# Kernel optimization log

Hardware: AMD Instinct MI355X
Metric: run time of the kernel (lower is better)

The kernel has to match this reference:

```python
import jax, jax.numpy as jnp
import numpy as np

B, H, S, D = 65536, 512, 256, 64  # batch, hidden_dim, memory_slots, slot_size


def setup_inputs() -> dict:
    key = jax.random.key(0)
    ks = jax.random.split(key, 8)
    scale = 1.0 / np.sqrt(H)
    return {
        "query": jax.random.normal(ks[0], (B, H), jnp.float32),
        "content": jax.random.normal(ks[1], (B, H), jnp.float32),
        "memory": jax.random.normal(ks[2], (S, D), jnp.float32),
        "memory_age": jax.random.uniform(ks[3], (S,), jnp.float32, 0.0, 30.0),
        "W_read": jax.random.normal(ks[4], (H, S), jnp.float32) * scale,
        "b_read": jnp.zeros((S,), jnp.float32),
        "W_write": jax.random.normal(ks[5], (H, S), jnp.float32) * scale,
        "b_write": jnp.zeros((S,), jnp.float32),
        "W_content": jax.random.normal(ks[6], (H, D), jnp.float32) * scale,
        "b_content": jnp.zeros((D,), jnp.float32),
    }


def reference(query, content, memory, memory_age,
              W_read, b_read, W_write, b_write, W_content, b_content):
    # ---- read: attention-based addressing over memory slots ----
    read_weights = jax.nn.softmax(query @ W_read + b_read, axis=-1)      # [B, S]
    read_content = read_weights @ memory                                  # [B, D]

    # ---- write: consolidation dynamics (vectorized per-slot EMA) ----
    write_weights = jax.nn.softmax(query @ W_write + b_write, axis=-1)   # [B, S]
    processed_content = content @ W_content + b_content                   # [B, D]
    w_mean = write_weights.mean(axis=0)                                    # [S]
    c_mean = processed_content.mean(axis=0)                                # [D]

    active = w_mean > 0.01                                                 # [S] bool
    consolidation = jax.nn.sigmoid(memory_age * 0.1)                       # [S]
    # effective blend factor; zero for inactive slots (slot left untouched)
    alpha = jnp.where(active, w_mean * consolidation, 0.0)[:, None]        # [S, 1]
    new_memory = (1.0 - alpha) * memory + alpha * c_mean[None, :]          # [S, D]
    new_age = memory_age + active.astype(memory_age.dtype)                 # [S]

    return read_content, new_memory, new_age
```

## Files before the change

kernel.cpp:

```cpp
#include <hip/hip_runtime.h>
#include <hip/hip_bf16.h>


typedef short short8 __attribute__((ext_vector_type(8)));
typedef float floatx4 __attribute__((ext_vector_type(4)));

#define H_DIM 512
#define BM 32

#define WS_WT    0
#define WS_MEMT  589824
#define WS_BFULL 622592
#define WS_WSUM  624896
#define WS_CSUM  625920

__device__ __forceinline__ unsigned short f2b(float f) {
  unsigned u = __float_as_uint(f);
  u += 0x7fffu + ((u >> 16) & 1u);
  return (unsigned short)(u >> 16);
}
__device__ __forceinline__ float b2f(unsigned short h) {
  return __uint_as_float(((unsigned)h) << 16);
}
__device__ __forceinline__ unsigned cvt2(float x, float y) {
  union { __hip_bfloat162 h; unsigned u; } c;
  c.h = __float22bfloat162_rn(make_float2(x, y));
  return c.u;
}

__global__ void drcn_init(const float* __restrict__ W_read, const float* __restrict__ W_write,
                          const float* __restrict__ W_content, const float* __restrict__ b_read,
                          const float* __restrict__ b_write, const float* __restrict__ b_content,
                          const float* __restrict__ memory,
                          unsigned short* __restrict__ Wt, unsigned short* __restrict__ memT,
                          float* __restrict__ bfull, float* __restrict__ w_sum,
                          float* __restrict__ c_sum) {
  int idx = blockIdx.x * 256 + threadIdx.x;
  if (idx < 294912) {
    int n = idx >> 9, k = idx & 511;
    float v;
    if (n < 256)      v = W_read[k * 256 + n];
    else if (n < 512) v = W_write[k * 256 + (n - 256)];
    else              v = W_content[k * 64 + (n - 512)];
    Wt[idx] = f2b(v);
  } else if (idx < 311296) {
    int i = idx - 294912;
    int d = i >> 8, s = i & 255;
    memT[i] = f2b(memory[s * 64 + d]);
  } else if (idx < 311872) {
    int n = idx - 311296;
    bfull[n] = (n < 256) ? b_read[n] : (n < 512 ? b_write[n - 256] : b_content[n - 512]);
  } else if (idx < 312192) {
    int i = idx - 311872;
    if (i < 256) w_sum[i] = 0.0f; else c_sum[i - 256] = 0.0f;
  }
}

__global__ __launch_bounds__(256, 2) void drcn_main(
    const float* __restrict__ query, const float* __restrict__ content,
    const unsigned short* __restrict__ Wt, const float* __restrict__ bfull,
    const unsigned short* __restrict__ memT, float* __restrict__ w_sum,
    float* __restrict__ c_sum, float* __restrict__ out) {
  __shared__ __align__(16) char smem[65536];
  unsigned short* lg = (unsigned short*)smem;
  float* cs = (float*)(smem + 37376);
  float* cp = (float*)(smem + 38400);

  const int t = threadIdx.x;
  const int wv = t >> 6;
  const int ln = t & 63;
  const int ln15 = ln & 15;
  const int quad = ln >> 4;
  const int m0 = blockIdx.x * BM;

  const unsigned short* bp[9];
  short8 breg[9];
  #pragma unroll
  for (int j = 0; j < 9; j++) {
    bp[j] = Wt + (size_t)(((wv * 9 + j) * 16 + ln15) * 512 + quad * 8);
    breg[j] = *(const short8*)bp[j];
  }

  float bias[9];
  #pragma unroll
  for (int j = 0; j < 9; j++) bias[j] = bfull[(wv * 9 + j) * 16 + ln15];

  {
    const int row = t >> 3, jj = t & 7;
    const float* qrow = query   + (size_t)(m0 + row) * H_DIM;
    const float* crow = content + (size_t)(m0 + row) * H_DIM;
    char* aqr = smem + row * 1024;
    char* acr = smem + 32768 + row * 1024;
    #pragma unroll
    for (int i = 0; i < 8; i++) {
      const int g = jj + i * 8;
      const int sw = ((g ^ (row & 7)) << 4);
      float4 f0 = *(const float4*)(qrow + g * 8);
      float4 f1 = *(const float4*)(qrow + g * 8 + 4);
      float4 g0 = *(const float4*)(crow + g * 8);
      float4 g1 = *(const float4*)(crow + g * 8 + 4);
      short8 s; unsigned* su = (unsigned*)&s;
      su[0] = cvt2(f0.x, f0.y); su[1] = cvt2(f0.z, f0.w);
      su[2] = cvt2(f1.x, f1.y); su[3] = cvt2(f1.z, f1.w);
      *(short8*)(aqr + sw) = s;
      short8 sc; unsigned* cu = (unsigned*)&sc;
      cu[0] = cvt2(g0.x, g0.y); cu[1] = cvt2(g0.z, g0.w);
      cu[2] = cvt2(g1.x, g1.y); cu[3] = cvt2(g1.z, g1.w);
      *(short8*)(acr + sw) = sc;
    }
  }

  floatx4 acc[2][9];
  #pragma unroll
  for (int mt = 0; mt < 2; mt++)
    #pragma unroll
    for (int j = 0; j < 9; j++) {
      floatx4 z = {0.0f, 0.0f, 0.0f, 0.0f};
      acc[mt][j] = z;
    }

  __syncthreads();

  #pragma unroll 2
  for (int it = 0; it < 16; ++it) {
    short8 aq[2], ac[2];
    #pragma unroll
    for (int mt = 0; mt < 2; mt++) {
      const int row = mt * 16 + ln15;
      const int sw = row * 1024 + ((((it * 4 + quad) ^ (row & 7))) << 4);
      aq[mt] = *(const short8*)(smem + sw);
      ac[mt] = *(const short8*)(smem + 32768 + sw);
    }
    #pragma unroll
    for (int j = 0; j < 9; j++) {
      const int nt = wv * 9 + j;
      #pragma unroll
      for (int mt = 0; mt < 2; mt++) {
        short8 a = (nt >= 32) ? ac[mt] : aq[mt];
        acc[mt][j] = __builtin_amdgcn_mfma_f32_16x16x32_bf16(a, breg[j], acc[mt][j], 0, 0, 0);
      }
      if (it < 15)
        breg[j] = *(const short8*)(bp[j] + (it + 1) * 32);
    }
  }
  __syncthreads();

  #pragma unroll
  for (int j = 0; j < 9; j++) {
    int n = (wv * 9 + j) * 16 + ln15;
    #pragma unroll
    for (int mt = 0; mt < 2; mt++) {
      #pragma unroll
      for (int r = 0; r < 4; r++) {
        int row = mt * 16 + quad * 4 + r;
        lg[row * 584 + n] = f2b(acc[mt][j][r] + bias[j]);
      }
    }
  }
  cs[t] = 0.0f;
  if (t < 64) cp[t] = 0.0f;
  __syncthreads();

  const int r = t >> 3, c = t & 7;
  unsigned short* lrow = lg + r * 584;

  {
    float v[32];
    #pragma unroll
    for (int ch = 0; ch < 4; ch++) {
      short8 u = *(const short8*)(lrow + c * 32 + ch * 8);
      #pragma unroll
      for (int e = 0; e < 8; e++) v[ch * 8 + e] = b2f((unsigned short)u[e]);
    }
    float mx = -3.0e38f;
    #pragma unroll
    for (int i = 0; i < 32; i++) mx = fmaxf(mx, v[i]);
    mx = fmaxf(mx, __shfl_xor(mx, 1));
    mx = fmaxf(mx, __shfl_xor(mx, 2));
    mx = fmaxf(mx, __shfl_xor(mx, 4));
    float sm = 0.0f;
    #pragma unroll
    for (int i = 0; i < 32; i++) { v[i] = __expf(v[i] - mx); sm += v[i]; }
    sm += __shfl_xor(sm, 1);
    sm += __shfl_xor(sm, 2);
    sm += __shfl_xor(sm, 4);
    float inv = 1.0f / sm;
    #pragma unroll
    for (int ch = 0; ch < 4; ch++) {
      short8 u;
      #pragma unroll
      for (int e = 0; e < 8; e++) u[e] = (short)f2b(v[ch * 8 + e] * inv);
      *(short8*)(lrow + c * 32 + ch * 8) = u;
    }
  }
  {
    float v[32];
    #pragma unroll
    for (int ch = 0; ch < 4; ch++) {
      short8 u = *(const short8*)(lrow + 256 + c * 32 + ch * 8);
      #pragma unroll
      for (int e = 0; e < 8; e++) v[ch * 8 + e] = b2f((unsigned short)u[e]);
    }
    float mx = -3.0e38f;
    #pragma unroll
    for (int i = 0; i < 32; i++) mx = fmaxf(mx, v[i]);
    mx = fmaxf(mx, __shfl_xor(mx, 1));
    mx = fmaxf(mx, __shfl_xor(mx, 2));
    mx = fmaxf(mx, __shfl_xor(mx, 4));
    float sm = 0.0f;
    #pragma unroll
    for (int i = 0; i < 32; i++) { v[i] = __expf(v[i] - mx); sm += v[i]; }
    sm += __shfl_xor(sm, 1);
    sm += __shfl_xor(sm, 2);
    sm += __shfl_xor(sm, 4);
    float inv = 1.0f / sm;
    #pragma unroll
    for (int i = 0; i < 32; i++) {
      float p = v[i] * inv;
      p += __shfl_xor(p, 8);
      p += __shfl_xor(p, 16);
      p += __shfl_xor(p, 32);
      v[i] = p;
    }
    if (ln < 8) {
      #pragma unroll
      for (int i = 0; i < 32; i++) atomicAdd(&cs[c * 32 + i], v[i]);
    }
  }
  {
    float v[8];
    short8 u = *(const short8*)(lrow + 512 + c * 8);
    #pragma unroll
    for (int e = 0; e < 8; e++) v[e] = b2f((unsigned short)u[e]);
    #pragma unroll
    for (int e = 0; e < 8; e++) {
      float p = v[e];
      p += __shfl_xor(p, 8);
      p += __shfl_xor(p, 16);
      p += __shfl_xor(p, 32);
      v[e] = p;
    }
    if (ln < 8) {
      #pragma unroll
      for (int e = 0; e < 8; e++) atomicAdd(&cp[c * 8 + e], v[e]);
    }
  }
  __syncthreads();

  {
    int mt = wv & 1, nd0 = (wv >> 1) * 2;
    floatx4 ra[2];
    floatx4 z = {0.0f, 0.0f, 0.0f, 0.0f};
    ra[0] = z; ra[1] = z;
    #pragma unroll
    for (int ks = 0; ks < 8; ks++) {
      int s0 = ks * 32 + quad * 8;
      short8 a = *(const short8*)(lg + (mt * 16 + ln15) * 584 + s0);
      #pragma unroll
      for (int dt = 0; dt < 2; dt++) {
        short8 b = *(const short8*)(memT + ((nd0 + dt) * 16 + ln15) * 256 + s0);
        ra[dt] = __builtin_amdgcn_mfma_f32_16x16x32_bf16(a, b, ra[dt], 0, 0, 0);
      }
    }
    #pragma unroll
    for (int dt = 0; dt < 2; dt++)
      #pragma unroll
      for (int rr = 0; rr < 4; rr++) {
        int orow = m0 + mt * 16 + quad * 4 + rr;
        out[(size_t)orow * 64 + (nd0 + dt) * 16 + ln15] = ra[dt][rr];
      }
  }

  atomicAdd(&w_sum[t], cs[t]);
  if (t < 64) atomicAdd(&c_sum[t], cp[t]);
}

__global__ void drcn_final(const float* __restrict__ memory, const float* __restrict__ age,
                           const float* __restrict__ w_sum, const float* __restrict__ c_sum,
                           float* __restrict__ out_mem, float* __restrict__ out_age) {
  int idx = blockIdx.x * 256 + threadIdx.x;
  int s = idx >> 6, d = idx & 63;
  float wm = w_sum[s] * (1.0f / 65536.0f);
  bool act = wm > 0.01f;
  float cons = 1.0f / (1.0f + __expf(-age[s] * 0.1f));
  float alpha = act ? wm * cons : 0.0f;
  float cm = c_sum[d] * (1.0f / 65536.0f);
  out_mem[idx] = (1.0f - alpha) * memory[idx] + alpha * cm;
  if (d == 0) out_age[s] = age[s] + (act ? 1.0f : 0.0f);
}

extern "C" void kernel_launch(void* const* d_in, const int* in_sizes, int n_in,
                              void* d_out, int out_size, void* d_ws, size_t ws_size,
                              hipStream_t stream) {
  (void)in_sizes; (void)n_in; (void)out_size; (void)ws_size;
  const float* query     = (const float*)d_in[0];
  const float* content   = (const float*)d_in[1];
  const float* memory    = (const float*)d_in[2];
  const float* mem_age   = (const float*)d_in[3];
  const float* W_read    = (const float*)d_in[4];
  const float* b_read    = (const float*)d_in[5];
  const float* W_write   = (const float*)d_in[6];
  const float* b_write   = (const float*)d_in[7];
  const float* W_content = (const float*)d_in[8];
  const float* b_content = (const float*)d_in[9];
  float* out = (float*)d_out;
  char* ws = (char*)d_ws;
  unsigned short* Wt   = (unsigned short*)(ws + WS_WT);
  unsigned short* memT = (unsigned short*)(ws + WS_MEMT);
  float* bfull = (float*)(ws + WS_BFULL);
  float* w_sum = (float*)(ws + WS_WSUM);
  float* c_sum = (float*)(ws + WS_CSUM);

  drcn_init<<<1220, 256, 0, stream>>>(W_read, W_write, W_content, b_read, b_write,
                                      b_content, memory, Wt, memT, bfull, w_sum, c_sum);
  drcn_main<<<2048, 256, 0, stream>>>(query, content, Wt, bfull, memT, w_sum, c_sum, out);
  drcn_final<<<64, 256, 0, stream>>>(memory, mem_age, w_sum, c_sum,
                                     out + 4194304, out + 4210688);
}
```

Before: 420.4 us.

## Stage A operand in two K-halves to shrink LDS and raise occupancy

Instead of staging the full 512-wide bf16 query and content rows into 64KB of shared memory, the kernel now stages each 256-wide K half into the same 32KB region. Query and content for a row are interleaved within each row slot, and a sync separates the two passes. Shared memory drops to about 38KB and launch bounds go from 2 to 4 blocks per CU, so more waves can hide global-load and MFMA latency. The cost is an extra barrier plus a global-load phase in the middle of the MFMA loop. The tighter register budget may also cause spills, given the 72 accumulator registers.

```diff
diff --git a/kernel.cpp b/kernel.cpp
--- a/kernel.cpp
+++ b/kernel.cpp
@@ -4,6 +4,7 @@
 
 typedef short short8 __attribute__((ext_vector_type(8)));
 typedef float floatx4 __attribute__((ext_vector_type(4)));
+typedef unsigned uintx2 __attribute__((ext_vector_type(2)));
 
 #define H_DIM 512
 #define BM 32
@@ -56,12 +57,12 @@
   }
 }
 
-__global__ __launch_bounds__(256, 2) void drcn_main(
+__global__ __launch_bounds__(256, 4) void drcn_main(
     const float* __restrict__ query, const float* __restrict__ content,
     const unsigned short* __restrict__ Wt, const float* __restrict__ bfull,
     const unsigned short* __restrict__ memT, float* __restrict__ w_sum,
     float* __restrict__ c_sum, float* __restrict__ out) {
-  __shared__ __align__(16) char smem[65536];
+  __shared__ __align__(16) char smem[38912];
   unsigned short* lg = (unsigned short*)smem;
   float* cs = (float*)(smem + 37376);
   float* cp = (float*)(smem + 38400);
@@ -85,31 +86,6 @@
   #pragma unroll
   for (int j = 0; j < 9; j++) bias[j] = bfull[(wv * 9 + j) * 16 + ln15];
 
-  {
-    const int row = t >> 3, jj = t & 7;
-    const float* qrow = query   + (size_t)(m0 + row) * H_DIM;
-    const float* crow = content + (size_t)(m0 + row) * H_DIM;
-    char* aqr = smem + row * 1024;
-    char* acr = smem + 32768 + row * 1024;
-    #pragma unroll
-    for (int i = 0; i < 8; i++) {
-      const int g = jj + i * 8;
-      const int sw = ((g ^ (row & 7)) << 4);
-      float4 f0 = *(const float4*)(qrow + g * 8);
-      float4 f1 = *(const float4*)(qrow + g * 8 + 4);
-      float4 g0 = *(const float4*)(crow + g * 8);
-      float4 g1 = *(const float4*)(crow + g * 8 + 4);
-      short8 s; unsigned* su = (unsigned*)&s;
-      su[0] = cvt2(f0.x, f0.y); su[1] = cvt2(f0.z, f0.w);
-      su[2] = cvt2(f1.x, f1.y); su[3] = cvt2(f1.z, f1.w);
-      *(short8*)(aqr + sw) = s;
-      short8 sc; unsigned* cu = (unsigned*)&sc;
-      cu[0] = cvt2(g0.x, g0.y); cu[1] = cvt2(g0.z, g0.w);
-      cu[2] = cvt2(g1.x, g1.y); cu[3] = cvt2(g1.z, g1.w);
-      *(short8*)(acr + sw) = sc;
-    }
-  }
-
   floatx4 acc[2][9];
   #pragma unroll
   for (int mt = 0; mt < 2; mt++)
@@ -119,31 +95,51 @@
       acc[mt][j] = z;
     }
 
-  __syncthreads();
-
-  #pragma unroll 2
-  for (int it = 0; it < 16; ++it) {
-    short8 aq[2], ac[2];
-    #pragma unroll
-    for (int mt = 0; mt < 2; mt++) {
-      const int row = mt * 16 + ln15;
-      const int sw = row * 1024 + ((((it * 4 + quad) ^ (row & 7))) << 4);
-      aq[mt] = *(const short8*)(smem + sw);
-      ac[mt] = *(const short8*)(smem + 32768 + sw);
-    }
-    #pragma unroll
-    for (int j = 0; j < 9; j++) {
-      const int nt = wv * 9 + j;
+  const int row = t >> 3, jj = t & 7;
+  const float* qrow = query   + (size_t)(m0 + row) * H_DIM;
+  const float* crow = content + (size_t)(m0 + row) * H_DIM;
+  char* abase = smem + row * 1024;
+
+  #pragma unroll
+  for (int h = 0; h < 2; h++) {
+    #pragma unroll
+    for (int i = 0; i < 8; i++) {
+      const int fi = i * 8 + jj;
+      const int sw = (((fi >> 1) ^ (row & 7)) << 4) + (fi & 1) * 8;
+      float4 fq = *(const float4*)(qrow + h * 256 + fi * 4);
+      float4 fc = *(const float4*)(crow + h * 256 + fi * 4);
+      uintx2 q2 = { cvt2(fq.x, fq.y), cvt2(fq.z, fq.w) };
+      uintx2 c2 = { cvt2(fc.x, fc.y), cvt2(fc.z, fc.w) };
+      *(uintx2*)(abase + sw) = q2;
+      *(uintx2*)(abase + 512 + sw) = c2;
+    }
+    __syncthreads();
+
+    #pragma unroll 2
+    for (int it8 = 0; it8 < 8; ++it8) {
+      const int it = h * 8 + it8;
+      short8 aq[2], ac[2];
       #pragma unroll
       for (int mt = 0; mt < 2; mt++) {
-        short8 a = (nt >= 32) ? ac[mt] : aq[mt];
-        acc[mt][j] = __builtin_amdgcn_mfma_f32_16x16x32_bf16(a, breg[j], acc[mt][j], 0, 0, 0);
-      }
-      if (it < 15)
-        breg[j] = *(const short8*)(bp[j] + (it + 1) * 32);
-    }
-  }
-  __syncthreads();
+        const int ar = mt * 16 + ln15;
+        const int sw = ar * 1024 + ((((it8 * 4 + quad) ^ (ar & 7))) << 4);
+        aq[mt] = *(const short8*)(smem + sw);
+        ac[mt] = *(const short8*)(smem + sw + 512);
+      }
+      #pragma unroll
+      for (int j = 0; j < 9; j++) {
+        const int nt = wv * 9 + j;
+        #pragma unroll
+        for (int mt = 0; mt < 2; mt++) {
+          short8 a = (nt >= 32) ? ac[mt] : aq[mt];
+          acc[mt][j] = __builtin_amdgcn_mfma_f32_16x16x32_bf16(a, breg[j], acc[mt][j], 0, 0, 0);
+        }
+        if (it < 15)
+          breg[j] = *(const short8*)(bp[j] + (it + 1) * 32);
+      }
+    }
+    __syncthreads();
+  }
 
   #pragma unroll
   for (int j = 0; j < 9; j++) {
@@ -152,8 +148,8 @@
     for (int mt = 0; mt < 2; mt++) {
       #pragma unroll
       for (int r = 0; r < 4; r++) {
-        int row = mt * 16 + quad * 4 + r;
-        lg[row * 584 + n] = f2b(acc[mt][j][r] + bias[j]);
+        int rr = mt * 16 + quad * 4 + r;
+        lg[rr * 584 + n] = f2b(acc[mt][j][r] + bias[j]);
       }
     }
   }
```

Result: slower. 655.6 us (+55.9%).
